# Performance work log

Hardware: AMD Instinct MI355X
Metric: run time of the kernel (lower is better)

The kernel has to match this reference:

```python
import jax, jax.numpy as jnp
import numpy as np

# EEACSF hyperparameters (module defaults)
CUTOFF = 5.2
ANG_CUTOFF = 3.5
RADIAL_ETA = 16.0
ANGULAR_ETA = 8.0
RDIV = 16          # radial_dist_divisions
ADIV = 4           # angular_dist_divisions
ZETA = 32.0
SECTIONS = 4       # angle_sections
R_START = 0.8
A_START = 0.8
N_SPECIES = 87     # size of periodic-table / valence table

N_ATOMS = 20000
N_EDGES = 640000       # radial edges
N_ANG_EDGES = 160000   # angular-graph edges
N_PAIRS = 560000       # angle pairs


def setup_inputs() -> dict:
    key = jax.random.key(0)
    ks = jax.random.split(key, 12)
    species = jax.random.randint(ks[0], (N_ATOMS,), 0, N_SPECIES)
    # radial graph: distances in (R_START, CUTOFF)
    distances = R_START + (CUTOFF - R_START) * jax.random.uniform(ks[1], (N_EDGES,), jnp.float32)
    switch = jax.random.uniform(ks[2], (N_EDGES,), jnp.float32)
    edge_src = jax.random.randint(ks[3], (N_EDGES,), 0, N_ATOMS)
    edge_dst = jax.random.randint(ks[4], (N_EDGES,), 0, N_ATOMS)
    # angular graph
    ang_angles = np.pi * jax.random.uniform(ks[5], (N_PAIRS,), jnp.float32)
    ang_distances = A_START + (ANG_CUTOFF - A_START) * jax.random.uniform(ks[6], (N_ANG_EDGES,), jnp.float32)
    ang_switch = jax.random.uniform(ks[7], (N_ANG_EDGES,), jnp.float32)
    ang_edge_dst = jax.random.randint(ks[8], (N_ANG_EDGES,), 0, N_ATOMS)
    angle_src = jax.random.randint(ks[9], (N_PAIRS,), 0, N_ANG_EDGES)
    angle_dst = jax.random.randint(ks[10], (N_PAIRS,), 0, N_ANG_EDGES)
    central_atom = jax.random.randint(ks[11], (N_PAIRS,), 0, N_ATOMS)
    # valence structure table (stands in for the preprocessed VALENCE_STRUCTURE constant)
    valence_table = jax.random.uniform(jax.random.fold_in(key, 99), (N_SPECIES, 4), jnp.float32)
    return {
        "species": species, "distances": distances, "switch": switch,
        "edge_src": edge_src, "edge_dst": edge_dst,
        "ang_angles": ang_angles, "ang_distances": ang_distances,
        "ang_switch": ang_switch, "ang_edge_dst": ang_edge_dst,
        "angle_src": angle_src, "angle_dst": angle_dst,
        "central_atom": central_atom, "valence_table": valence_table,
    }


def reference(species, distances, switch, edge_src, edge_dst,
              ang_angles, ang_distances, ang_switch, ang_edge_dst,
              angle_src, angle_dst, central_atom, valence_table):
    n_atoms = species.shape[0]
    valence = valence_table[species]                                  # [N,4]

    # ---- radial AEV ----
    shiftR = jnp.asarray(np.linspace(R_START, CUTOFF, RDIV + 1)[None, :-1], distances.dtype)
    x2 = RADIAL_ETA * (distances[:, None] - shiftR) ** 2              # [E,16]
    radial_terms = 0.25 * jnp.exp(-x2) * switch[:, None]              # [E,16]
    radial_aev = jax.ops.segment_sum(
        radial_terms[:, :, None] * valence[edge_dst, None, :],        # [E,16,4]
        edge_src, num_segments=n_atoms,
    ).reshape(n_atoms, -1)                                            # [N,64]

    # ---- angular AEV ----
    d12 = 0.5 * (ang_distances[angle_src] + ang_distances[angle_dst])[:, None]  # [P,1]
    angle_start = np.pi / (2 * SECTIONS)
    shiftZ = jnp.asarray((np.linspace(0, np.pi, SECTIONS + 1) + angle_start)[None, :-1], ang_distances.dtype)
    shiftA = jnp.asarray(np.linspace(A_START, ANG_CUTOFF, ADIV + 1)[None, :-1], ang_distances.dtype)
    factor1 = (0.5 + 0.5 * jnp.cos(ang_angles[:, None] - shiftZ)) ** ZETA       # [P,4]
    factor2 = jnp.exp(-ANGULAR_ETA * (d12 - shiftA) ** 2)                       # [P,4]
    angular_terms = (factor1[:, None, :] * factor2[:, :, None]).reshape(-1, SECTIONS * ADIV)
    angular_terms = angular_terms * 2 * (ang_switch[angle_src] * ang_switch[angle_dst])[:, None]  # [P,16]

    valence_dst = valence[ang_edge_dst]                               # [E2,4]
    vp = valence_dst[angle_src] + valence_dst[angle_dst]              # [P,4]
    vm = valence_dst[angle_src] * valence_dst[angle_dst]              # [P,4]
    valence_ang = (vp[:, :, None] * vm[:, None, :]).reshape(-1, 16)   # [P,16]

    angular_aev = jax.ops.segment_sum(
        angular_terms[:, :, None] * valence_ang[:, None, :],          # [P,16,16]
        central_atom, num_segments=n_atoms,
    ).reshape(n_atoms, -1)                                            # [N,256]

    onehot = jax.nn.one_hot(species, N_SPECIES, dtype=distances.dtype)  # [N,87]
    return jnp.concatenate((onehot, radial_aev, angular_aev), axis=-1)  # [N,407]
```

## Files before the change

kernel.cpp:

```cpp
#include <hip/hip_runtime.h>
#include <hip/hip_fp16.h>
#include <math.h>

#define NCOLS   407
#define RAD_OFF 87
#define ANG_OFF 151
#define T1      3072
#define WB      32
#define MAXBKT  640
#define CAPF    1792


typedef __attribute__((ext_vector_type(8))) _Float16 f16x8;
typedef __attribute__((ext_vector_type(4))) float    f32x4;

static __device__ inline unsigned pack2(float a, float b) {
    __half2 h = __floats2half2_rn(a, b);
    return *reinterpret_cast<unsigned*>(&h);
}
static __device__ inline float2 unpack2(unsigned u) {
    __half2 h = *reinterpret_cast<__half2*>(&u);
    return __half22float2(h);
}

__global__ __launch_bounds__(256) void pass0_kernel(const int* __restrict__ esrc,
                                                    const int* __restrict__ central,
                                                    const float* __restrict__ ang_dist,
                                                    const float* __restrict__ ang_sw,
                                                    const int* __restrict__ ang_edge_dst,
                                                    const int* __restrict__ species,
                                                    const float4* __restrict__ valence,
                                                    int* __restrict__ tileHist,
                                                    uint4* __restrict__ edata,
                                                    int n_edges, int n_pairs, int n_ang_edges,
                                                    int nbkt, int nt_rad, int nt_ang) {
    int bid = blockIdx.x;
    int t = threadIdx.x;

    if (bid < nt_rad + nt_ang) {
        __shared__ int lh[MAXBKT];
        int is_ang = bid >= nt_rad;
        const int* key = is_ang ? central : esrc;
        int n   = is_ang ? n_pairs : n_edges;
        int off = (is_ang ? bid - nt_rad : bid) * T1;
        for (int b = t; b < nbkt; b += 256) lh[b] = 0;
        __syncthreads();
        #pragma unroll
        for (int k = 0; k < T1 / 256; ++k) {
            int i = off + k * 256 + t;
            if (i < n) atomicAdd(&lh[key[i] >> 5], 1);
        }
        __syncthreads();
        int* row = tileHist + (size_t)bid * nbkt;
        for (int b = t; b < nbkt; b += 256) row[b] = lh[b];
        return;
    }

    int i = (bid - nt_rad - nt_ang) * 2560 + t;
    #pragma unroll
    for (int k = 0; k < 10; ++k, i += 256) {
        if (i < n_ang_edges) {
            float4 v = valence[species[ang_edge_dst[i]]];
            uint4 r;
            r.x = __float_as_uint(ang_dist[i]);
            r.y = __float_as_uint(ang_sw[i]);
            r.z = pack2(v.x, v.y);
            r.w = pack2(v.z, v.w);
            edata[i] = r;
        }
    }
}

__global__ __launch_bounds__(256) void scanA_kernel(int* __restrict__ tileHist,
                                                    int* __restrict__ bktTotals,
                                                    int nt_rad, int nt_ang, int nbkt) {
    int wid  = blockIdx.x * 4 + (threadIdx.x >> 6);
    int lane = threadIdx.x & 63;
    if (wid >= 2 * nbkt) return;
    int g = wid >= nbkt;
    int b = g ? wid - nbkt : wid;
    int* th = tileHist + (g ? (size_t)nt_rad * nbkt : 0);
    int nt = g ? nt_ang : nt_rad;
    int run = 0;
    for (int k0 = 0; k0 < nt; k0 += 64) {
        int k = k0 + lane;
        int v = (k < nt) ? th[(size_t)k * nbkt + b] : 0;
        int s = v;
        #pragma unroll
        for (int o = 1; o < 64; o <<= 1) {
            int u = __shfl_up(s, o, 64);
            if (lane >= o) s += u;
        }
        if (k < nt) th[(size_t)k * nbkt + b] = run + s - v;
        run += __shfl(s, 63, 64);
    }
    if (lane == 0) bktTotals[g * MAXBKT + b] = run;
}

__global__ __launch_bounds__(1024) void scanB_kernel(const int* __restrict__ bktTotals,
                                                     int* __restrict__ bktBase, int nbkt) {
    int g = blockIdx.x;
    const int* tot = bktTotals + g * MAXBKT;
    int* bb = bktBase + g * (MAXBKT + 1);
    __shared__ int part[1024];
    int t = threadIdx.x;
    int v = (t < nbkt) ? tot[t] : 0;
    part[t] = v;
    __syncthreads();
    for (int o = 1; o < 1024; o <<= 1) {
        int u = (t >= o) ? part[t - o] : 0;
        __syncthreads();
        part[t] += u;
        __syncthreads();
    }
    if (t < nbkt) bb[t] = part[t] - v;
    if (t == nbkt - 1) bb[nbkt] = part[t];
}

__global__ __launch_bounds__(256) void pass1_kernel(
    const float* __restrict__ dist, const float* __restrict__ sw,
    const int* __restrict__ esrc, const int* __restrict__ edst,
    const float* __restrict__ ang_angles,
    const int* __restrict__ psrc, const int* __restrict__ pdst,
    const int* __restrict__ central,
    const int* __restrict__ species, const float4* __restrict__ valence,
    const int* __restrict__ tileHist, const int* __restrict__ bktBase,
    uint4* __restrict__ arr_rad, uint4* __restrict__ arr_ang,
    int n_edges, int n_pairs, int nbkt, int nt_rad)
{
    __shared__ uint4 buf[T1];
    __shared__ int   dst[T1];
    __shared__ int   lh[MAXBKT];
    __shared__ int   gb[MAXBKT];
    __shared__ int   sc[256];

    int bid = blockIdx.x;
    int t = threadIdx.x;
    int is_ang = bid >= nt_rad;
    const int* key = is_ang ? central : esrc;
    int n   = is_ang ? n_pairs : n_edges;
    int off = (is_ang ? bid - nt_rad : bid) * T1;
    int cnt = min(T1, n - off);
    uint4* arr = is_ang ? arr_ang : arr_rad;
    const int* row = tileHist + (size_t)bid * nbkt;
    const int* bb  = bktBase + is_ang * (MAXBKT + 1);

    for (int b = t; b < nbkt; b += 256) { lh[b] = 0; gb[b] = row[b] + bb[b]; }
    __syncthreads();

    int meta[T1 / 256];
    #pragma unroll
    for (int k = 0; k < T1 / 256; ++k) {
        int i = off + k * 256 + t;
        meta[k] = -1;
        if (i < n) {
            int b = key[i] >> 5;
            int r = atomicAdd(&lh[b], 1);
            meta[k] = (b << 12) | r;
        }
    }
    __syncthreads();

    {
        int ch = (nbkt + 255) >> 8;
        int vals[4];
        int lo = t * ch, s = 0;
        for (int k = 0; k < ch; ++k) {
            int idx = lo + k;
            int v = (idx < nbkt) ? lh[idx] : 0;
            vals[k] = v; s += v;
        }
        sc[t] = s;
        __syncthreads();
        for (int o = 1; o < 256; o <<= 1) {
            int v = (t >= o) ? sc[t - o] : 0;
            __syncthreads();
            sc[t] += v;
            __syncthreads();
        }
        int run = sc[t] - s;
        for (int k = 0; k < ch; ++k) {
            int idx = lo + k;
            if (idx < nbkt) lh[idx] = run;
            run += vals[k];
        }
        __syncthreads();
    }

    #pragma unroll
    for (int k = 0; k < T1 / 256; ++k) {
        if (meta[k] < 0) continue;
        int i = off + k * 256 + t;
        int b = meta[k] >> 12, r = meta[k] & 4095;
        uint4 rec;
        if (!is_ang) {
            float d  = dist[i];
            float ps = 0.25f * sw[i];
            float4 v = valence[species[edst[i]]];
            rec.x = __float_as_uint(d);
            rec.y = pack2(ps * v.x, ps * v.y);
            rec.z = pack2(ps * v.z, ps * v.w);
            rec.w = (unsigned)esrc[i];
        } else {
            rec.x = (unsigned)psrc[i];
            rec.y = (unsigned)pdst[i];
            rec.z = __float_as_uint(ang_angles[i]);
            rec.w = (unsigned)central[i];
        }
        int pos = lh[b] + r;
        buf[pos] = rec;
        dst[pos] = gb[b] + r;
    }
    __syncthreads();

    #pragma unroll
    for (int k = 0; k < T1 / 256; ++k) {
        int j = k * 256 + t;
        if (j < cnt) arr[dst[j]] = buf[j];
    }
}

__global__ __launch_bounds__(256) void pass2B_kernel(
    const uint4* __restrict__ arr_rad, const uint4* __restrict__ arr_ang,
    const uint4* __restrict__ edata,
    const int* __restrict__ bktBase,
    const int* __restrict__ species,
    float* __restrict__ out, int nbkt, int n_atoms)
{
    __shared__ uint4 buf[CAPF];
    __shared__ unsigned short ord[CAPF];
    __shared__ int lh[WB];
    __shared__ int sA[WB + 1];
    __shared__ uint4 stg[4][256];

    int bid = blockIdx.x;
    int t = threadIdx.x;
    int g = bid >= nbkt;
    int b = g ? bid - nbkt : bid;
    const int* bb = bktBase + g * (MAXBKT + 1);
    int lo  = bb[b];
    int cnt = min(bb[b + 1] - lo, CAPF);
    const uint4* arr = g ? arr_ang : arr_rad;
    int loA = b << 5;

    if (t < WB) lh[t] = 0;
    __syncthreads();
    for (int j = t; j < cnt; j += 256) {
        uint4 r = arr[lo + j];
        buf[j] = r;
        atomicAdd(&lh[(int)r.w - loA], 1);
    }
    __syncthreads();
    if (t == 0) {
        int run = 0;
        for (int a = 0; a < WB; ++a) { sA[a] = run; run += lh[a]; }
        sA[WB] = run;
    }
    __syncthreads();
    if (t < WB) lh[t] = sA[t];
    __syncthreads();
    for (int j = t; j < cnt; j += 256) {
        int a = (int)buf[j].w - loA;
        int pos = atomicAdd(&lh[a], 1);
        ord[pos] = (unsigned short)j;
    }
    __syncthreads();

    int w    = t >> 6;
    int lane = t & 63;
    int m  = lane & 15;
    int g4 = lane >> 4;

    if (g) {
        const _Float16* hl = (const _Float16*)stg[w];
        for (int ai = 0; ai < 8; ++ai) {
            int a = w * 8 + ai;
            int atom = loA + a;
            if (atom >= n_atoms) break;
            int beg = sA[a], end = sA[a + 1];
            f32x4 acc = {0.f, 0.f, 0.f, 0.f};

            for (int base = beg; base < end; base += 64) {
                int idx = base + lane;
                unsigned q[16];
                if (idx < end) {
                    uint4 pr = buf[ord[idx]];
                    int e1 = (int)pr.x;
                    int e2 = (int)pr.y;
                    float ang = __uint_as_float(pr.z);
                    uint4 r1 = edata[e1];
                    uint4 r2 = edata[e2];
                    float d12 = 0.5f * (__uint_as_float(r1.x) + __uint_as_float(r2.x));
                    float swp = 2.0f * __uint_as_float(r1.y) * __uint_as_float(r2.y);
                    float2 v1a = unpack2(r1.z), v1b = unpack2(r1.w);
                    float2 v2a = unpack2(r2.z), v2b = unpack2(r2.w);
                    float vp[4] = {v1a.x + v2a.x, v1a.y + v2a.y, v1b.x + v2b.x, v1b.y + v2b.y};
                    float vm[4] = {v1a.x * v2a.x, v1a.y * v2a.y, v1b.x * v2b.x, v1b.y * v2b.y};

                    float sa, ca;
                    __sincosf(ang, &sa, &ca);
                    const float czv[4] = { 0.92387953f,  0.38268343f, -0.38268343f, -0.92387953f };
                    const float szv[4] = { 0.38268343f,  0.92387953f,  0.92387953f,  0.38268343f };
                    float f1v[4];
                    #pragma unroll
                    for (int z = 0; z < 4; ++z) {
                        float y = 0.5f + 0.5f * (ca * czv[z] + sa * szv[z]);
                        float y2 = y * y, y4 = y2 * y2, y8 = y4 * y4, y16 = y8 * y8;
                        f1v[z] = y16 * y16;
                    }
                    float f2sv[4];
                    #pragma unroll
                    for (int aa = 0; aa < 4; ++aa) {
                        float x = d12 - (0.8f + 0.675f * (float)aa);
                        f2sv[aa] = swp * __expf(-8.0f * x * x);
                    }
                    #pragma unroll
                    for (int aa = 0; aa < 4; ++aa) {
                        q[aa * 2 + 0] = pack2(f2sv[aa] * f1v[0], f2sv[aa] * f1v[1]);
                        q[aa * 2 + 1] = pack2(f2sv[aa] * f1v[2], f2sv[aa] * f1v[3]);
                    }
                    #pragma unroll
                    for (int i2 = 0; i2 < 4; ++i2) {
                        q[8 + i2 * 2 + 0] = pack2(vp[i2] * vm[0], vp[i2] * vm[1]);
                        q[8 + i2 * 2 + 1] = pack2(vp[i2] * vm[2], vp[i2] * vm[3]);
                    }
                } else {
                    #pragma unroll
                    for (int k = 0; k < 16; ++k) q[k] = 0u;
                }
                stg[w][lane * 4 + 0] = make_uint4(q[0],  q[1],  q[2],  q[3]);
                stg[w][lane * 4 + 1] = make_uint4(q[4],  q[5],  q[6],  q[7]);
                stg[w][lane * 4 + 2] = make_uint4(q[8],  q[9],  q[10], q[11]);
                stg[w][lane * 4 + 3] = make_uint4(q[12], q[13], q[14], q[15]);
                asm volatile("s_waitcnt lgkmcnt(0)" ::: "memory");

                int cc = min(64, end - base);
                {
                    f16x8 wf, uf;
                    #pragma unroll
                    for (int i = 0; i < 8; ++i) {
                        int row = (g4 << 3) + i;
                        wf[i] = hl[row * 32 + m];
                        uf[i] = hl[row * 32 + 16 + m];
                    }
                    acc = __builtin_amdgcn_mfma_f32_16x16x32_f16(wf, uf, acc, 0, 0, 0);
                }
                if (cc > 32) {
                    f16x8 wf, uf;
                    #pragma unroll
                    for (int i = 0; i < 8; ++i) {
                        int row = 32 + (g4 << 3) + i;
                        wf[i] = hl[row * 32 + m];
                        uf[i] = hl[row * 32 + 16 + m];
                    }
                    acc = __builtin_amdgcn_mfma_f32_16x16x32_f16(wf, uf, acc, 0, 0, 0);
                }
                asm volatile("s_waitcnt lgkmcnt(0)" ::: "memory");
            }
            float* orow = out + (size_t)atom * NCOLS + ANG_OFF;
            #pragma unroll
            for (int r = 0; r < 4; ++r)
                orow[(g4 * 4 + r) * 16 + m] = acc[r];
        }
        return;
    }

    const _Float16* hl = (const _Float16*)buf;
    const float*    fl = (const float*)buf;
    float shiftm = 0.8f + 0.275f * (float)m;
    for (int ai = 0; ai < 8; ++ai) {
        int a = w * 8 + ai;
        int atom = loA + a;
        if (atom >= n_atoms) break;
        int beg = sA[a], end = sA[a + 1];
        f32x4 acc = {0.f, 0.f, 0.f, 0.f};

        for (int base = beg; base < end; base += 64) {
            int cnt2 = min(64, end - base);
            {
                f16x8 wf, uf;
                #pragma unroll
                for (int i = 0; i < 8; ++i) {
                    int k = (g4 << 3) + i;
                    int live = (k < cnt2);
                    int o = live ? (int)ord[base + k] : 0;
                    float d = fl[o * 4];
                    float x = d - shiftm;
                    float e = __expf(-16.0f * x * x);
                    wf[i] = live ? (_Float16)e : (_Float16)0.0f;
                    uf[i] = (live && m < 4) ? hl[o * 8 + 2 + m] : (_Float16)0.0f;
                }
                acc = __builtin_amdgcn_mfma_f32_16x16x32_f16(wf, uf, acc, 0, 0, 0);
            }
            if (cnt2 > 32) {
                f16x8 wf, uf;
                #pragma unroll
                for (int i = 0; i < 8; ++i) {
                    int k = 32 + (g4 << 3) + i;
                    int live = (k < cnt2);
                    int o = live ? (int)ord[base + k] : 0;
                    float d = fl[o * 4];
                    float x = d - shiftm;
                    float e = __expf(-16.0f * x * x);
                    wf[i] = live ? (_Float16)e : (_Float16)0.0f;
                    uf[i] = (live && m < 4) ? hl[o * 8 + 2 + m] : (_Float16)0.0f;
                }
                acc = __builtin_amdgcn_mfma_f32_16x16x32_f16(wf, uf, acc, 0, 0, 0);
            }
        }
        if (m < 4) {
            size_t rowbase = (size_t)atom * NCOLS;
            #pragma unroll
            for (int r = 0; r < 4; ++r)
                out[rowbase + RAD_OFF + (g4 * 4 + r) * 4 + m] = acc[r];
        }
    }

    for (int idx2 = t; idx2 < WB * 87; idx2 += 256) {
        int a = idx2 / 87, c = idx2 - a * 87;
        int atom = loA + a;
        if (atom < n_atoms)
            out[(size_t)atom * NCOLS + c] = (c == species[atom]) ? 1.0f : 0.0f;
    }
}

extern "C" void kernel_launch(void* const* d_in, const int* in_sizes, int n_in,
                              void* d_out, int out_size, void* d_ws, size_t ws_size,
                              hipStream_t stream) {
    const int*   species      = (const int*)  d_in[0];
    const float* distances    = (const float*)d_in[1];
    const float* switch_      = (const float*)d_in[2];
    const int*   edge_src     = (const int*)  d_in[3];
    const int*   edge_dst     = (const int*)  d_in[4];
    const float* ang_angles   = (const float*)d_in[5];
    const float* ang_dist     = (const float*)d_in[6];
    const float* ang_switch   = (const float*)d_in[7];
    const int*   ang_edge_dst = (const int*)  d_in[8];
    const int*   angle_src    = (const int*)  d_in[9];
    const int*   angle_dst    = (const int*)  d_in[10];
    const int*   central_atom = (const int*)  d_in[11];
    const float4* valence     = (const float4*)d_in[12];

    float* out = (float*)d_out;

    const int n_atoms     = in_sizes[0];
    const int n_edges     = in_sizes[1];
    const int n_ang_edges = in_sizes[6];
    const int n_pairs     = in_sizes[5];

    const int nbkt   = (n_atoms + WB - 1) / WB;
    const int nt_rad = (n_edges + T1 - 1) / T1;
    const int nt_ang = (n_pairs + T1 - 1) / T1;

    char* ws = (char*)d_ws;
    size_t off = 0;
    auto alloc = [&](size_t bytes) -> void* {
        void* p = ws + off;
        off = (off + bytes + 15) & ~(size_t)15;
        return p;
    };
    uint4*  arr_rad     = (uint4*) alloc((size_t)n_edges * 16);
    uint4*  arr_ang     = (uint4*) alloc((size_t)n_pairs * 16);
    uint4*  edata       = (uint4*) alloc((size_t)n_ang_edges * 16);
    int*    tileHist    = (int*)   alloc((size_t)(nt_rad + nt_ang) * nbkt * 4);
    int*    bktTotals   = (int*)   alloc((size_t)2 * MAXBKT * sizeof(int));
    int*    bktBase     = (int*)   alloc((size_t)2 * (MAXBKT + 1) * sizeof(int));

    int nb_edata = (n_ang_edges + 2559) / 2560;
    pass0_kernel<<<nt_rad + nt_ang + nb_edata, 256, 0, stream>>>(
        edge_src, central_atom, ang_dist, ang_switch, ang_edge_dst,
        species, valence, tileHist, edata,
        n_edges, n_pairs, n_ang_edges, nbkt, nt_rad, nt_ang);

    scanA_kernel<<<(2 * nbkt + 3) / 4, 256, 0, stream>>>(
        tileHist, bktTotals, nt_rad, nt_ang, nbkt);

    scanB_kernel<<<2, 1024, 0, stream>>>(bktTotals, bktBase, nbkt);

    pass1_kernel<<<nt_rad + nt_ang, 256, 0, stream>>>(
        distances, switch_, edge_src, edge_dst,
        ang_angles, angle_src, angle_dst, central_atom,
        species, valence, tileHist, bktBase, arr_rad, arr_ang,
        n_edges, n_pairs, nbkt, nt_rad);

    pass2B_kernel<<<2 * nbkt, 256, 0, stream>>>(
        arr_rad, arr_ang, edata, bktBase, species, out, nbkt, n_atoms);
}
```

Measured before the change: 79.90 us.

## Replace histogram and scan passes with fixed-capacity buckets and atomic cursors

Result: slower. 81.74 us (+2.3%).

```diff
diff --git a/kernel.cpp b/kernel.cpp
--- a/kernel.cpp
+++ b/kernel.cpp
@@ -23,40 +23,21 @@
     return __half22float2(h);
 }
 
-__global__ __launch_bounds__(256) void pass0_kernel(const int* __restrict__ esrc,
-                                                    const int* __restrict__ central,
-                                                    const float* __restrict__ ang_dist,
-                                                    const float* __restrict__ ang_sw,
-                                                    const int* __restrict__ ang_edge_dst,
-                                                    const int* __restrict__ species,
-                                                    const float4* __restrict__ valence,
-                                                    int* __restrict__ tileHist,
-                                                    uint4* __restrict__ edata,
-                                                    int n_edges, int n_pairs, int n_ang_edges,
-                                                    int nbkt, int nt_rad, int nt_ang) {
+__global__ __launch_bounds__(256) void ze_kernel(const float* __restrict__ ang_dist,
+                                                 const float* __restrict__ ang_sw,
+                                                 const int* __restrict__ ang_edge_dst,
+                                                 const int* __restrict__ species,
+                                                 const float4* __restrict__ valence,
+                                                 uint4* __restrict__ edata,
+                                                 int* __restrict__ cursors,
+                                                 int n_ang_edges, int nb_edata) {
     int bid = blockIdx.x;
     int t = threadIdx.x;
-
-    if (bid < nt_rad + nt_ang) {
-        __shared__ int lh[MAXBKT];
-        int is_ang = bid >= nt_rad;
-        const int* key = is_ang ? central : esrc;
-        int n   = is_ang ? n_pairs : n_edges;
-        int off = (is_ang ? bid - nt_rad : bid) * T1;
-        for (int b = t; b < nbkt; b += 256) lh[b] = 0;
-        __syncthreads();
-        #pragma unroll
-        for (int k = 0; k < T1 / 256; ++k) {
-            int i = off + k * 256 + t;
-            if (i < n) atomicAdd(&lh[key[i] >> 5], 1);
-        }
-        __syncthreads();
-        int* row = tileHist + (size_t)bid * nbkt;
-        for (int b = t; b < nbkt; b += 256) row[b] = lh[b];
+    if (bid == nb_edata) {
+        for (int i = t; i < 2 * MAXBKT; i += 256) cursors[i] = 0;
         return;
     }
-
-    int i = (bid - nt_rad - nt_ang) * 2560 + t;
+    int i = bid * 2560 + t;
     #pragma unroll
     for (int k = 0; k < 10; ++k, i += 256) {
         if (i < n_ang_edges) {
@@ -71,52 +52,6 @@
     }
 }
 
-__global__ __launch_bounds__(256) void scanA_kernel(int* __restrict__ tileHist,
-                                                    int* __restrict__ bktTotals,
-                                                    int nt_rad, int nt_ang, int nbkt) {
-    int wid  = blockIdx.x * 4 + (threadIdx.x >> 6);
-    int lane = threadIdx.x & 63;
-    if (wid >= 2 * nbkt) return;
-    int g = wid >= nbkt;
-    int b = g ? wid - nbkt : wid;
-    int* th = tileHist + (g ? (size_t)nt_rad * nbkt : 0);
-    int nt = g ? nt_ang : nt_rad;
-    int run = 0;
-    for (int k0 = 0; k0 < nt; k0 += 64) {
-        int k = k0 + lane;
-        int v = (k < nt) ? th[(size_t)k * nbkt + b] : 0;
-        int s = v;
-        #pragma unroll
-        for (int o = 1; o < 64; o <<= 1) {
-            int u = __shfl_up(s, o, 64);
-            if (lane >= o) s += u;
-        }
-        if (k < nt) th[(size_t)k * nbkt + b] = run + s - v;
-        run += __shfl(s, 63, 64);
-    }
-    if (lane == 0) bktTotals[g * MAXBKT + b] = run;
-}
-
-__global__ __launch_bounds__(1024) void scanB_kernel(const int* __restrict__ bktTotals,
-                                                     int* __restrict__ bktBase, int nbkt) {
-    int g = blockIdx.x;
-    const int* tot = bktTotals + g * MAXBKT;
-    int* bb = bktBase + g * (MAXBKT + 1);
-    __shared__ int part[1024];
-    int t = threadIdx.x;
-    int v = (t < nbkt) ? tot[t] : 0;
-    part[t] = v;
-    __syncthreads();
-    for (int o = 1; o < 1024; o <<= 1) {
-        int u = (t >= o) ? part[t - o] : 0;
-        __syncthreads();
-        part[t] += u;
-        __syncthreads();
-    }
-    if (t < nbkt) bb[t] = part[t] - v;
-    if (t == nbkt - 1) bb[nbkt] = part[t];
-}
-
 __global__ __launch_bounds__(256) void pass1_kernel(
     const float* __restrict__ dist, const float* __restrict__ sw,
     const int* __restrict__ esrc, const int* __restrict__ edst,
@@ -124,7 +59,7 @@
     const int* __restrict__ psrc, const int* __restrict__ pdst,
     const int* __restrict__ central,
     const int* __restrict__ species, const float4* __restrict__ valence,
-    const int* __restrict__ tileHist, const int* __restrict__ bktBase,
+    int* __restrict__ cur_rad, int* __restrict__ cur_ang,
     uint4* __restrict__ arr_rad, uint4* __restrict__ arr_ang,
     int n_edges, int n_pairs, int nbkt, int nt_rad)
 {
@@ -138,14 +73,13 @@
     int t = threadIdx.x;
     int is_ang = bid >= nt_rad;
     const int* key = is_ang ? central : esrc;
+    int* cursor = is_ang ? cur_ang : cur_rad;
     int n   = is_ang ? n_pairs : n_edges;
     int off = (is_ang ? bid - nt_rad : bid) * T1;
     int cnt = min(T1, n - off);
     uint4* arr = is_ang ? arr_ang : arr_rad;
-    const int* row = tileHist + (size_t)bid * nbkt;
-    const int* bb  = bktBase + is_ang * (MAXBKT + 1);
-
-    for (int b = t; b < nbkt; b += 256) { lh[b] = 0; gb[b] = row[b] + bb[b]; }
+
+    for (int b = t; b < nbkt; b += 256) lh[b] = 0;
     __syncthreads();
 
     int meta[T1 / 256];
@@ -164,9 +98,9 @@
     {
         int ch = (nbkt + 255) >> 8;
         int vals[4];
-        int lo = t * ch, s = 0;
+        int lo2 = t * ch, s = 0;
         for (int k = 0; k < ch; ++k) {
-            int idx = lo + k;
+            int idx = lo2 + k;
             int v = (idx < nbkt) ? lh[idx] : 0;
             vals[k] = v; s += v;
         }
@@ -180,8 +114,12 @@
         }
         int run = sc[t] - s;
         for (int k = 0; k < ch; ++k) {
-            int idx = lo + k;
-            if (idx < nbkt) lh[idx] = run;
+            int idx = lo2 + k;
+            if (idx < nbkt) {
+                lh[idx] = run;
+                if (vals[k] > 0)
+                    gb[idx] = idx * CAPF + atomicAdd(&cursor[idx], vals[k]);
+            }
             run += vals[k];
         }
         __syncthreads();
@@ -207,23 +145,27 @@
             rec.z = __float_as_uint(ang_angles[i]);
             rec.w = (unsigned)central[i];
         }
-        int pos = lh[b] + r;
+        int pos  = lh[b] + r;
+        int gpos = gb[b] + r;
         buf[pos] = rec;
-        dst[pos] = gb[b] + r;
+        dst[pos] = (gpos < (b + 1) * CAPF) ? gpos : -1;
     }
     __syncthreads();
 
     #pragma unroll
     for (int k = 0; k < T1 / 256; ++k) {
         int j = k * 256 + t;
-        if (j < cnt) arr[dst[j]] = buf[j];
+        if (j < cnt) {
+            int d2 = dst[j];
+            if (d2 >= 0) arr[d2] = buf[j];
+        }
     }
 }
 
 __global__ __launch_bounds__(256) void pass2B_kernel(
     const uint4* __restrict__ arr_rad, const uint4* __restrict__ arr_ang,
     const uint4* __restrict__ edata,
-    const int* __restrict__ bktBase,
+    const int* __restrict__ cur_rad, const int* __restrict__ cur_ang,
     const int* __restrict__ species,
     float* __restrict__ out, int nbkt, int n_atoms)
 {
@@ -237,9 +179,8 @@
     int t = threadIdx.x;
     int g = bid >= nbkt;
     int b = g ? bid - nbkt : bid;
-    const int* bb = bktBase + g * (MAXBKT + 1);
-    int lo  = bb[b];
-    int cnt = min(bb[b + 1] - lo, CAPF);
+    int lo  = b * CAPF;
+    int cnt = min(g ? cur_ang[b] : cur_rad[b], CAPF);
     const uint4* arr = g ? arr_ang : arr_rad;
     int loA = b << 5;
 
@@ -248,7 +189,8 @@
     for (int j = t; j < cnt; j += 256) {
         uint4 r = arr[lo + j];
         buf[j] = r;
-        atomicAdd(&lh[(int)r.w - loA], 1);
+        int a = (int)r.w - loA;
+        if ((unsigned)a < WB) atomicAdd(&lh[a], 1);
     }
     __syncthreads();
     if (t == 0) {
@@ -261,8 +203,10 @@
     __syncthreads();
     for (int j = t; j < cnt; j += 256) {
         int a = (int)buf[j].w - loA;
-        int pos = atomicAdd(&lh[a], 1);
-        ord[pos] = (unsigned short)j;
+        if ((unsigned)a < WB) {
+            int pos = atomicAdd(&lh[a], 1);
+            ord[pos] = (unsigned short)j;
+        }
     }
     __syncthreads();
 
@@ -459,30 +403,24 @@
         off = (off + bytes + 15) & ~(size_t)15;
         return p;
     };
-    uint4*  arr_rad     = (uint4*) alloc((size_t)n_edges * 16);
-    uint4*  arr_ang     = (uint4*) alloc((size_t)n_pairs * 16);
-    uint4*  edata       = (uint4*) alloc((size_t)n_ang_edges * 16);
-    int*    tileHist    = (int*)   alloc((size_t)(nt_rad + nt_ang) * nbkt * 4);
-    int*    bktTotals   = (int*)   alloc((size_t)2 * MAXBKT * sizeof(int));
-    int*    bktBase     = (int*)   alloc((size_t)2 * (MAXBKT + 1) * sizeof(int));
+    uint4* arr_rad = (uint4*)alloc((size_t)nbkt * CAPF * 16);
+    uint4* arr_ang = (uint4*)alloc((size_t)nbkt * CAPF * 16);
+    uint4* edata   = (uint4*)alloc((size_t)n_ang_edges * 16);
+    int*   cursors = (int*)  alloc((size_t)2 * MAXBKT * sizeof(int));
+    int* cur_rad = cursors;
+    int* cur_ang = cursors + MAXBKT;
 
     int nb_edata = (n_ang_edges + 2559) / 2560;
-    pass0_kernel<<<nt_rad + nt_ang + nb_edata, 256, 0, stream>>>(
-        edge_src, central_atom, ang_dist, ang_switch, ang_edge_dst,
-        species, valence, tileHist, edata,
-        n_edges, n_pairs, n_ang_edges, nbkt, nt_rad, nt_ang);
-
-    scanA_kernel<<<(2 * nbkt + 3) / 4, 256, 0, stream>>>(
-        tileHist, bktTotals, nt_rad, nt_ang, nbkt);
-
-    scanB_kernel<<<2, 1024, 0, stream>>>(bktTotals, bktBase, nbkt);
+    ze_kernel<<<nb_edata + 1, 256, 0, stream>>>(
+        ang_dist, ang_switch, ang_edge_dst, species, valence,
+        edata, cursors, n_ang_edges, nb_edata);
 
     pass1_kernel<<<nt_rad + nt_ang, 256, 0, stream>>>(
         distances, switch_, edge_src, edge_dst,
         ang_angles, angle_src, angle_dst, central_atom,
-        species, valence, tileHist, bktBase, arr_rad, arr_ang,
+        species, valence, cur_rad, cur_ang, arr_rad, arr_ang,
         n_edges, n_pairs, nbkt, nt_rad);
 
     pass2B_kernel<<<2 * nbkt, 256, 0, stream>>>(
-        arr_rad, arr_ang, edata, bktBase, species, out, nbkt, n_atoms);
-}
+        arr_rad, arr_ang, edata, cur_rad, cur_ang, species, out, nbkt, n_atoms);
+}
```
